# Performance work log

Measured on AMD Instinct MI355X. Metric: run time of the kernel, lower is better.

The kernel has to match this reference:

```python
import jax, jax.numpy as jnp
import numpy as np

PROJ_DIM = 8192
INPUT_DIM = 512
THRESH = 1e-08


def _signed_sqrt(x):
    return jnp.sign(x) * jnp.sqrt(jnp.abs(x))


def _make_sketch_matrix(key, input_dim, proj_dim):
    kh, ks = jax.random.split(key)
    h = jax.random.randint(kh, (input_dim,), 0, proj_dim)
    s = jnp.sign(jax.random.uniform(ks, (input_dim,), minval=-1.0, maxval=1.0)).astype(jnp.float32)
    M = jnp.zeros((input_dim, proj_dim), dtype=jnp.float32)
    return M.at[jnp.arange(input_dim), h].set(s)


def setup_inputs() -> dict:
    key = jax.random.key(0)
    kx, k1, k2 = jax.random.split(key, 3)
    x = jax.random.normal(kx, (32, 14, 14, INPUT_DIM), dtype=jnp.float32)
    M1 = _make_sketch_matrix(k1, INPUT_DIM, PROJ_DIM)
    M2 = _make_sketch_matrix(k2, INPUT_DIM, PROJ_DIM)
    return {"x": x, "M1": M1, "M2": M2}


def reference(x, M1, M2):
    B, H, W, C = x.shape
    x_flat = x.reshape(-1, C)                      # [B*H*W, C]
    # count-sketch projections (dense matmul, as in the original layer)
    p1 = (x_flat @ M1).astype(jnp.complex64)       # [B*H*W, P]
    p2 = (x_flat @ M2).astype(jnp.complex64)
    # circular convolution via FFT
    sketch = jnp.fft.fft(p1, axis=-1) * jnp.fft.fft(p2, axis=-1)
    y = jnp.real(jnp.fft.ifft(sketch, axis=-1)).astype(jnp.float32)
    y = y.reshape(B, H, W, -1).sum(axis=(1, 2))    # sum-pool over spatial dims -> [B, P]
    y = _signed_sqrt(y)
    # tf.nn.l2_normalize(x, axis=1, epsilon=1e-10)
    inv_norm = jax.lax.rsqrt(jnp.maximum(jnp.sum(y * y, axis=1, keepdims=True), 1e-10))
    return y * inv_norm
```

## Files before the change

### kernel.cpp

```cpp
#include <hip/hip_runtime.h>
#include <math.h>

#define PROJ 8192
#define CDIM 512
#define HWPOS 196
#define NBATCH 32
#define NSLAB 7
#define NSEG 16

typedef __attribute__((ext_vector_type(8))) short   short8;
typedef __attribute__((ext_vector_type(4))) float   f32x4;

__device__ __forceinline__ unsigned short f2bf(float f) {
    unsigned u = __float_as_uint(f);
    u += 0x7fff + ((u >> 16) & 1);
    return (unsigned short)(u >> 16);
}
__device__ __forceinline__ float bf2f(unsigned short h) {
    return __uint_as_float(((unsigned)h) << 16);
}

__device__ __forceinline__ void lds_uadd(unsigned* p, unsigned v) {
    __attribute__((address_space(3))) unsigned* lp =
        (__attribute__((address_space(3))) unsigned*)p;
    asm volatile("ds_add_u32 %0, %1" : : "v"(lp), "v"(v) : "memory");
}
__device__ __forceinline__ unsigned lds_uadd_rtn(unsigned* p, unsigned v) {
    __attribute__((address_space(3))) unsigned* lp =
        (__attribute__((address_space(3))) unsigned*)p;
    unsigned r;
    asm volatile("ds_add_rtn_u32 %0, %1, %2\n\ts_waitcnt lgkmcnt(0)"
                 : "=v"(r) : "v"(lp), "v"(v) : "memory");
    return r;
}

#define BI_PACK 0x2110002110003210ULL
#define BJ_PACK 0x3323213323213210ULL

__device__ __forceinline__ void seg_entry(int seg, int e,
    const int* __restrict__ h1, const float* __restrict__ s1,
    const int* __restrict__ h2, const float* __restrict__ s2,
    int& bin, int& sg)
{
    const int bi = (int)((BI_PACK >> (seg * 4)) & 15);
    const int bj = (int)((BJ_PACK >> (seg * 4)) & 15);
    const int r = e >> 7, c = e & 127;
    int gi, gj;
    if (seg < 10) { gi = bi * 128 + r; gj = bj * 128 + c; }
    else          { gi = bj * 128 + c; gj = bi * 128 + r; }
    bin = (h1[gi] + h2[gj]) & (PROJ - 1);
    sg  = (int)((__float_as_uint(s1[gi]) ^ __float_as_uint(s2[gj])) >> 31);
}

__global__ __launch_bounds__(256) void extract_kernel(
    const float* __restrict__ M1, const float* __restrict__ M2,
    int* __restrict__ h1, float* __restrict__ s1,
    int* __restrict__ h2, float* __restrict__ s2,
    float* __restrict__ norm, float* __restrict__ pbins)
{
    const int row = blockIdx.x;
    const float* M = blockIdx.y ? M2 : M1;
    int*   h = blockIdx.y ? h2 : h1;
    float* s = blockIdx.y ? s2 : s1;
    const float* mrow = M + (size_t)row * PROJ;

    if (blockIdx.x == 0 && blockIdx.y == 0 && threadIdx.x < NBATCH)
        norm[threadIdx.x] = 0.0f;

    for (int i = threadIdx.x * 4; i < PROJ; i += 256 * 4) {
        float4 v = *(const float4*)(mrow + i);
        if (v.x != 0.0f) { h[row] = i + 0; s[row] = v.x; }
        if (v.y != 0.0f) { h[row] = i + 1; s[row] = v.y; }
        if (v.z != 0.0f) { h[row] = i + 2; s[row] = v.z; }
        if (v.w != 0.0f) { h[row] = i + 3; s[row] = v.w; }
    }

    const int bid = blockIdx.x * 2 + blockIdx.y;
    float* pz = pbins + (size_t)bid * 4096;
#pragma unroll
    for (int i = 0; i < 4; ++i)
        *(float4*)(pz + i * 1024 + threadIdx.x * 4) = make_float4(0.f, 0.f, 0.f, 0.f);
}

__global__ __launch_bounds__(256) void combo_kernel(
    const float* __restrict__ x,
    unsigned short* __restrict__ XThi, unsigned short* __restrict__ XTlo,
    const int* __restrict__ h1, const float* __restrict__ s1,
    const int* __restrict__ h2, const float* __restrict__ s2,
    unsigned* __restrict__ csr)
{
    __shared__ float    xt[32][513];
    __shared__ unsigned cnt[PROJ];
    __shared__ unsigned sc[256];
    const int tid = threadIdx.x;

    if (blockIdx.x < 224) {
        const int ks = blockIdx.x % NSLAB;
        const int bt = blockIdx.x / NSLAB;
        const float* xb = x + (size_t)bt * HWPOS * CDIM;
        const int k0 = ks * 32;
#pragma unroll
        for (int i = 0; i < 16; ++i) {
            const int idx = i * 1024 + tid * 4;
            const int kr  = idx >> 9;
            const int c   = idx & 511;
            float4 v = make_float4(0.f, 0.f, 0.f, 0.f);
            if (k0 + kr < HWPOS) v = *(const float4*)(xb + (size_t)(k0 + kr) * CDIM + c);
            xt[kr][c+0] = v.x; xt[kr][c+1] = v.y; xt[kr][c+2] = v.z; xt[kr][c+3] = v.w;
        }
        __syncthreads();

        unsigned short* ohi = XThi + ((size_t)bt * NSLAB + ks) * 16384;
        unsigned short* olo = XTlo + ((size_t)bt * NSLAB + ks) * 16384;
#pragma unroll
        for (int i = 0; i < 8; ++i) {
            const int ch   = i * 256 + tid;
            const int c16  = ch & 15;
            const int quad = (ch >> 4) & 3;
            const int cgrp = ch >> 6;
            const int c    = cgrp * 16 + c16;
            short8 vh, vl;
#pragma unroll
            for (int j = 0; j < 8; ++j) {
                float f = xt[quad * 8 + j][c];
                unsigned short h = f2bf(f);
                vh[j] = (short)h;
                vl[j] = (short)f2bf(f - bf2f(h));
            }
            *(short8*)(ohi + ch * 8) = vh;
            *(short8*)(olo + ch * 8) = vl;
        }
    } else {
        const int seg = blockIdx.x - 224;

        for (int i = tid; i < PROJ; i += 256) cnt[i] = 0u;
        __syncthreads();
#pragma unroll 8
        for (int k = 0; k < 64; ++k) {
            const int e = k * 256 + tid;
            int bin, sg;
            seg_entry(seg, e, h1, s1, h2, s2, bin, sg);
            lds_uadd(&cnt[bin], 1u);
        }
        __syncthreads();

        unsigned c[32]; unsigned tot = 0;
#pragma unroll
        for (int i = 0; i < 32; ++i) { c[i] = cnt[tid * 32 + i]; tot += c[i]; }
        sc[tid] = tot;
        __syncthreads();
        for (int off = 1; off < 256; off <<= 1) {
            unsigned v = (tid >= off) ? sc[tid - off] : 0u;
            __syncthreads();
            sc[tid] += v;
            __syncthreads();
        }
        unsigned base = sc[tid] - tot;
#pragma unroll
        for (int i = 0; i < 32; ++i) { unsigned t = c[i]; cnt[tid * 32 + i] = base; base += t; }
        __syncthreads();

        unsigned* cs = csr + (size_t)seg * 16384;
#pragma unroll 8
        for (int k = 0; k < 64; ++k) {
            const int e = k * 256 + tid;
            int bin, sg;
            seg_entry(seg, e, h1, s1, h2, s2, bin, sg);
            const unsigned pos = lds_uadd_rtn(&cnt[bin], 1u);
            cs[pos] = ((unsigned)bin << 15) | ((unsigned)sg << 14) | (unsigned)e;
        }
    }
}

__global__ __launch_bounds__(256) void gramgather_kernel(
    const unsigned short* __restrict__ XThi, const unsigned short* __restrict__ XTlo,
    const unsigned* __restrict__ csr, float* __restrict__ pbins)
{
    const int id  = blockIdx.x;
    const int sub = id >> 3;
    const int tp  = sub & 15;
    const int bat = (id & 7) + 8 * (sub >> 4);
    const int bi = (int)((BI_PACK >> (tp * 4)) & 15);
    const int bj = (int)((BJ_PACK >> (tp * 4)) & 15);

    const int tid  = threadIdx.x;
    const int w    = tid >> 6;
    const int lane = tid & 63;
    const int rowq = w >> 1, colq = w & 1;

    __shared__ __align__(16) unsigned short Sbuf[2][4][4096];

    const int tile = (w < 2) ? bi : bj;
    const unsigned short* srcbase = ((w & 1) ? XTlo : XThi)
                                  + (size_t)bat * NSLAB * 16384 + (size_t)tile * 4096;

    {
        const unsigned short* src = srcbase;
        unsigned short* dst = &Sbuf[0][w][0];
#pragma unroll
        for (int i = 0; i < 8; ++i)
            __builtin_amdgcn_global_load_lds(
                (const __attribute__((address_space(1))) void*)(src + i * 512 + lane * 8),
                (__attribute__((address_space(3))) void*)(dst + i * 512), 16, 0, 0);
    }

    float* page = pbins + ((size_t)bat * NSEG + tp) * PROJ;

    f32x4 acc[16];
#pragma unroll
    for (int i = 0; i < 16; ++i) { acc[i][0]=0.f; acc[i][1]=0.f; acc[i][2]=0.f; acc[i][3]=0.f; }

    for (int ks = 0; ks < NSLAB; ++ks) {
        __syncthreads();
        const int buf = ks & 1;

        if (ks + 1 < NSLAB) {
            const unsigned short* src = srcbase + (size_t)(ks + 1) * 16384;
            unsigned short* dst = &Sbuf[buf ^ 1][w][0];
#pragma unroll
            for (int i = 0; i < 8; ++i)
                __builtin_amdgcn_global_load_lds(
                    (const __attribute__((address_space(1))) void*)(src + i * 512 + lane * 8),
                    (__attribute__((address_space(3))) void*)(dst + i * 512), 16, 0, 0);
        }

        short8 ah[4], al[4], bh4[4], bl[4];
#pragma unroll
        for (int t = 0; t < 4; ++t) {
            ah[t]  = *(const short8*)&Sbuf[buf][0][(rowq * 4 + t) * 512 + lane * 8];
            al[t]  = *(const short8*)&Sbuf[buf][1][(rowq * 4 + t) * 512 + lane * 8];
            bh4[t] = *(const short8*)&Sbuf[buf][2][(colq * 4 + t) * 512 + lane * 8];
            bl[t]  = *(const short8*)&Sbuf[buf][3][(colq * 4 + t) * 512 + lane * 8];
        }
#pragma unroll
        for (int mt = 0; mt < 4; ++mt)
#pragma unroll
            for (int nt = 0; nt < 4; ++nt) {
                const int idx = mt * 4 + nt;
                acc[idx] = __builtin_amdgcn_mfma_f32_16x16x32_bf16(ah[mt], bh4[nt], acc[idx], 0, 0, 0);
                acc[idx] = __builtin_amdgcn_mfma_f32_16x16x32_bf16(ah[mt], bl[nt],  acc[idx], 0, 0, 0);
                acc[idx] = __builtin_amdgcn_mfma_f32_16x16x32_bf16(al[mt], bh4[nt], acc[idx], 0, 0, 0);
            }
    }

    __syncthreads();
    float* tileL = (float*)Sbuf;
    const int quad = lane >> 4;
#pragma unroll
    for (int mt = 0; mt < 4; ++mt)
#pragma unroll
        for (int reg = 0; reg < 4; ++reg) {
            const int rl = rowq * 64 + mt * 16 + quad * 4 + reg;
#pragma unroll
            for (int nt = 0; nt < 4; ++nt) {
                const int cl = colq * 64 + nt * 16 + (lane & 15);
                tileL[rl * 128 + cl] = acc[mt * 4 + nt][reg];
            }
        }
    __syncthreads();

    const uint4* ce = (const uint4*)(csr + (size_t)tp * 16384 + (size_t)tid * 64);
    uint4 E[16];
#pragma unroll
    for (int i = 0; i < 16; ++i) E[i] = ce[i];

    float a = 0.f;
    unsigned cur = E[0].x >> 15;
    bool first = true;
#pragma unroll
    for (int i = 0; i < 16; ++i) {
#pragma unroll
        for (int j = 0; j < 4; ++j) {
            const unsigned ent = (j == 0) ? E[i].x : (j == 1) ? E[i].y
                               : (j == 2) ? E[i].z : E[i].w;
            const unsigned b = ent >> 15;
            float v = tileL[ent & 0x3FFF];
            v = (ent & 0x4000u) ? -v : v;
            if (b != cur) {
                if (first) { unsafeAtomicAdd(&page[cur], a); first = false; }
                else       { page[cur] = a; }
                cur = b; a = v;
            } else {
                a += v;
            }
        }
    }
    unsafeAtomicAdd(&page[cur], a);
}

__global__ __launch_bounds__(256) void reduce_kernel(
    const float* __restrict__ pbins, float* __restrict__ out,
    float* __restrict__ norm)
{
    const int chunk = blockIdx.x;
    const int bat   = blockIdx.y;
    const int tid   = threadIdx.x;
    const int base  = chunk * 1024 + tid * 4;

    const float* pb = pbins + (size_t)bat * NSEG * PROJ;
    float4 v = make_float4(0.f, 0.f, 0.f, 0.f);
#pragma unroll
    for (int t = 0; t < NSEG; ++t) {
        float4 p = *(const float4*)(pb + (size_t)t * PROJ + base);
        v.x += p.x; v.y += p.y; v.z += p.z; v.w += p.w;
    }

    float4 sv;
    sv.x = (v.x >= 0.f) ? sqrtf(v.x) : -sqrtf(-v.x);
    sv.y = (v.y >= 0.f) ? sqrtf(v.y) : -sqrtf(-v.y);
    sv.z = (v.z >= 0.f) ? sqrtf(v.z) : -sqrtf(-v.z);
    sv.w = (v.w >= 0.f) ? sqrtf(v.w) : -sqrtf(-v.w);
    *(float4*)(out + (size_t)bat * PROJ + base) = sv;

    float local = fabsf(v.x) + fabsf(v.y) + fabsf(v.z) + fabsf(v.w);
#pragma unroll
    for (int off = 32; off > 0; off >>= 1) local += __shfl_down(local, off, 64);

    __shared__ float wred[4];
    if ((tid & 63) == 0) wred[tid >> 6] = local;
    __syncthreads();
    if (tid == 0)
        unsafeAtomicAdd(&norm[bat], wred[0] + wred[1] + wred[2] + wred[3]);
}

__global__ __launch_bounds__(256) void normalize_kernel(
    float* __restrict__ out, const float* __restrict__ norm)
{
    const int bat = blockIdx.y;
    const int idx = blockIdx.x * 1024 + threadIdx.x * 4;
    const float inv = rsqrtf(fmaxf(norm[bat], 1e-10f));
    float4* p = (float4*)(out + (size_t)bat * PROJ + idx);
    float4 v = *p;
    v.x *= inv; v.y *= inv; v.z *= inv; v.w *= inv;
    *p = v;
}

extern "C" void kernel_launch(void* const* d_in, const int* in_sizes, int n_in,
                              void* d_out, int out_size, void* d_ws, size_t ws_size,
                              hipStream_t stream)
{
    const float* x  = (const float*)d_in[0];
    const float* M1 = (const float*)d_in[1];
    const float* M2 = (const float*)d_in[2];
    float* out = (float*)d_out;

    char* ws = (char*)d_ws;
    int*            h1    = (int*)   (ws + 0);
    float*          s1    = (float*) (ws + 2048);
    int*            h2    = (int*)   (ws + 4096);
    float*          s2    = (float*) (ws + 6144);
    float*          norm  = (float*) (ws + 8192);
    unsigned*       csr   = (unsigned*)(ws + 16384);
    unsigned short* XThi  = (unsigned short*)(ws + 1064960);
    unsigned short* XTlo  = (unsigned short*)(ws + 8404992);
    float*          pbins = (float*) (ws + 15745024);

    extract_kernel<<<dim3(512, 2), 256, 0, stream>>>(M1, M2, h1, s1, h2, s2, norm, pbins);
    combo_kernel<<<240, 256, 0, stream>>>(x, XThi, XTlo, h1, s1, h2, s2, csr);
    gramgather_kernel<<<NSEG * NBATCH, 256, 0, stream>>>(XThi, XTlo, csr, pbins);
    reduce_kernel<<<dim3(8, NBATCH), 256, 0, stream>>>(pbins, out, norm);
    normalize_kernel<<<dim3(8, NBATCH), 256, 0, stream>>>(out, norm);
}
```

Before: 163.3 us.

## Fuse reduce and normalize into gram kernel via last-block-done counter

Removes the separate reduce and normalize launches. Each batch's sixteen segment blocks increment a per-batch done counter, and the last one to finish sums all segment pages, applies the signed sqrt, computes the norm and rescales the output in place. This saves two kernel launches and the global norm atomics, but the final reduction for each batch now runs on a single block after a serial tail, and it adds threadfence overhead to every block.

```diff
diff --git a/kernel.cpp b/kernel.cpp
--- a/kernel.cpp
+++ b/kernel.cpp
@@ -56,7 +56,7 @@
     const float* __restrict__ M1, const float* __restrict__ M2,
     int* __restrict__ h1, float* __restrict__ s1,
     int* __restrict__ h2, float* __restrict__ s2,
-    float* __restrict__ norm, float* __restrict__ pbins)
+    int* __restrict__ done, float* __restrict__ pbins)
 {
     const int row = blockIdx.x;
     const float* M = blockIdx.y ? M2 : M1;
@@ -65,7 +65,7 @@
     const float* mrow = M + (size_t)row * PROJ;
 
     if (blockIdx.x == 0 && blockIdx.y == 0 && threadIdx.x < NBATCH)
-        norm[threadIdx.x] = 0.0f;
+        done[threadIdx.x] = 0;
 
     for (int i = threadIdx.x * 4; i < PROJ; i += 256 * 4) {
         float4 v = *(const float4*)(mrow + i);
@@ -172,9 +172,10 @@
     }
 }
 
-__global__ __launch_bounds__(256) void gramgather_kernel(
+__global__ __launch_bounds__(256) void gramfin_kernel(
     const unsigned short* __restrict__ XThi, const unsigned short* __restrict__ XTlo,
-    const unsigned* __restrict__ csr, float* __restrict__ pbins)
+    const unsigned* __restrict__ csr, float* __restrict__ pbins,
+    float* __restrict__ out, int* __restrict__ done)
 {
     const int id  = blockIdx.x;
     const int sub = id >> 3;
@@ -189,6 +190,9 @@
     const int rowq = w >> 1, colq = w & 1;
 
     __shared__ __align__(16) unsigned short Sbuf[2][4][4096];
+    __shared__ int   lastflag;
+    __shared__ float wred[4];
+    __shared__ float sinv;
 
     const int tile = (w < 2) ? bi : bj;
     const unsigned short* srcbase = ((w & 1) ? XTlo : XThi)
@@ -286,53 +290,50 @@
         }
     }
     unsafeAtomicAdd(&page[cur], a);
-}
-
-__global__ __launch_bounds__(256) void reduce_kernel(
-    const float* __restrict__ pbins, float* __restrict__ out,
-    float* __restrict__ norm)
-{
-    const int chunk = blockIdx.x;
-    const int bat   = blockIdx.y;
-    const int tid   = threadIdx.x;
-    const int base  = chunk * 1024 + tid * 4;
+
+    __threadfence();
+    __syncthreads();
+    if (tid == 0)
+        lastflag = (atomicAdd(&done[bat], 1) == NSEG - 1);
+    __syncthreads();
+    if (!lastflag) return;
+    __threadfence();
 
     const float* pb = pbins + (size_t)bat * NSEG * PROJ;
-    float4 v = make_float4(0.f, 0.f, 0.f, 0.f);
-#pragma unroll
-    for (int t = 0; t < NSEG; ++t) {
-        float4 p = *(const float4*)(pb + (size_t)t * PROJ + base);
-        v.x += p.x; v.y += p.y; v.z += p.z; v.w += p.w;
-    }
-
-    float4 sv;
-    sv.x = (v.x >= 0.f) ? sqrtf(v.x) : -sqrtf(-v.x);
-    sv.y = (v.y >= 0.f) ? sqrtf(v.y) : -sqrtf(-v.y);
-    sv.z = (v.z >= 0.f) ? sqrtf(v.z) : -sqrtf(-v.z);
-    sv.w = (v.w >= 0.f) ? sqrtf(v.w) : -sqrtf(-v.w);
-    *(float4*)(out + (size_t)bat * PROJ + base) = sv;
-
-    float local = fabsf(v.x) + fabsf(v.y) + fabsf(v.z) + fabsf(v.w);
+    float* ob = out + (size_t)bat * PROJ;
+    float local = 0.f;
+#pragma unroll
+    for (int c = 0; c < 8; ++c) {
+        const int base = c * 1024 + tid * 4;
+        float4 v = make_float4(0.f, 0.f, 0.f, 0.f);
+#pragma unroll
+        for (int t = 0; t < NSEG; ++t) {
+            float4 p = *(const float4*)(pb + (size_t)t * PROJ + base);
+            v.x += p.x; v.y += p.y; v.z += p.z; v.w += p.w;
+        }
+        local += fabsf(v.x) + fabsf(v.y) + fabsf(v.z) + fabsf(v.w);
+        float4 sv;
+        sv.x = (v.x >= 0.f) ? sqrtf(v.x) : -sqrtf(-v.x);
+        sv.y = (v.y >= 0.f) ? sqrtf(v.y) : -sqrtf(-v.y);
+        sv.z = (v.z >= 0.f) ? sqrtf(v.z) : -sqrtf(-v.z);
+        sv.w = (v.w >= 0.f) ? sqrtf(v.w) : -sqrtf(-v.w);
+        *(float4*)(ob + base) = sv;
+    }
 #pragma unroll
     for (int off = 32; off > 0; off >>= 1) local += __shfl_down(local, off, 64);
-
-    __shared__ float wred[4];
     if ((tid & 63) == 0) wred[tid >> 6] = local;
     __syncthreads();
     if (tid == 0)
-        unsafeAtomicAdd(&norm[bat], wred[0] + wred[1] + wred[2] + wred[3]);
-}
-
-__global__ __launch_bounds__(256) void normalize_kernel(
-    float* __restrict__ out, const float* __restrict__ norm)
-{
-    const int bat = blockIdx.y;
-    const int idx = blockIdx.x * 1024 + threadIdx.x * 4;
-    const float inv = rsqrtf(fmaxf(norm[bat], 1e-10f));
-    float4* p = (float4*)(out + (size_t)bat * PROJ + idx);
-    float4 v = *p;
-    v.x *= inv; v.y *= inv; v.z *= inv; v.w *= inv;
-    *p = v;
+        sinv = rsqrtf(fmaxf(wred[0] + wred[1] + wred[2] + wred[3], 1e-10f));
+    __syncthreads();
+    const float inv = sinv;
+#pragma unroll
+    for (int c = 0; c < 8; ++c) {
+        const int base = c * 1024 + tid * 4;
+        float4 v = *(const float4*)(ob + base);
+        v.x *= inv; v.y *= inv; v.z *= inv; v.w *= inv;
+        *(float4*)(ob + base) = v;
+    }
 }
 
 extern "C" void kernel_launch(void* const* d_in, const int* in_sizes, int n_in,
@@ -349,15 +350,13 @@
     float*          s1    = (float*) (ws + 2048);
     int*            h2    = (int*)   (ws + 4096);
     float*          s2    = (float*) (ws + 6144);
-    float*          norm  = (float*) (ws + 8192);
+    int*            done  = (int*)   (ws + 8192);
     unsigned*       csr   = (unsigned*)(ws + 16384);
     unsigned short* XThi  = (unsigned short*)(ws + 1064960);
     unsigned short* XTlo  = (unsigned short*)(ws + 8404992);
     float*          pbins = (float*) (ws + 15745024);
 
-    extract_kernel<<<dim3(512, 2), 256, 0, stream>>>(M1, M2, h1, s1, h2, s2, norm, pbins);
+    extract_kernel<<<dim3(512, 2), 256, 0, stream>>>(M1, M2, h1, s1, h2, s2, done, pbins);
     combo_kernel<<<240, 256, 0, stream>>>(x, XThi, XTlo, h1, s1, h2, s2, csr);
-    gramgather_kernel<<<NSEG * NBATCH, 256, 0, stream>>>(XThi, XTlo, csr, pbins);
-    reduce_kernel<<<dim3(8, NBATCH), 256, 0, stream>>>(pbins, out, norm);
-    normalize_kernel<<<dim3(8, NBATCH), 256, 0, stream>>>(out, norm);
-}
+    gramfin_kernel<<<NSEG * NBATCH, 256, 0, stream>>>(XThi, XTlo, csr, pbins, out, done);
+}
```

Result: slower. 247.4 us (+51.5%).
